# Performance work log

Measured on AMD Instinct MI355X. Metric: run time of the kernel, lower is better.

The kernel has to match this reference:

```python
import jax, jax.numpy as jnp
import numpy as np

HEADS = 12
DIM_HEAD = 64
SCALE = DIM_HEAD ** -0.5


def setup_inputs() -> dict:
    key = jax.random.key(0)
    ks = jax.random.split(key, 7)
    b, n, dim = 16, 1024, 768
    inner = HEADS * DIM_HEAD
    x = jax.random.normal(ks[0], (b, n, dim), dtype=jnp.float32)
    Wq = jax.random.normal(ks[1], (dim, inner), dtype=jnp.float32) * (dim ** -0.5)
    Wkv = jax.random.normal(ks[2], (dim, 2 * inner), dtype=jnp.float32) * (dim ** -0.5)
    mix_pre = jax.random.normal(ks[3], (HEADS, HEADS), dtype=jnp.float32)
    mix_post = jax.random.normal(ks[4], (HEADS, HEADS), dtype=jnp.float32)
    Wo = jax.random.normal(ks[5], (inner, dim), dtype=jnp.float32) * (inner ** -0.5)
    bo = jnp.zeros((dim,), dtype=jnp.float32)
    return {"x": x, "Wq": Wq, "Wkv": Wkv, "mix_pre": mix_pre,
            "mix_post": mix_post, "Wo": Wo, "bo": bo}


def reference(x, Wq, Wkv, mix_pre, mix_post, Wo, bo):
    b, n, dim = x.shape
    h, d = HEADS, DIM_HEAD
    # projections (context is None -> context = x)
    q = (x @ Wq).reshape(b, n, h, d).transpose(0, 2, 1, 3)        # b h n d
    kv = x @ Wkv
    k = kv[..., : h * d].reshape(b, n, h, d).transpose(0, 2, 1, 3)
    v = kv[..., h * d:].reshape(b, n, h, d).transpose(0, 2, 1, 3)
    # scaled QK^T
    attn = jnp.einsum('bhid,bhjd->bhij', q, k) * SCALE             # b h n n
    # talking-heads pre-softmax: mix over head dim
    attn = jnp.einsum('bhij,hg->bgij', attn, mix_pre)
    attn = jax.nn.softmax(attn, axis=-1)
    # talking-heads post-softmax
    attn = jnp.einsum('bhij,hg->bgij', attn, mix_post)
    out = jnp.einsum('bhij,bhjd->bhid', attn, v)                   # b h n d
    out = out.transpose(0, 2, 1, 3).reshape(b, n, h * d)           # b n (h d)
    return out @ Wo + bo
```

## Files before the change

kernel.cpp:

```cpp
#include <hip/hip_runtime.h>


typedef _Float16 f16;
typedef _Float16 f16x8 __attribute__((ext_vector_type(8)));
typedef _Float16 f16x4 __attribute__((ext_vector_type(4)));
typedef float f32x4 __attribute__((ext_vector_type(4)));
typedef float fv4 __attribute__((ext_vector_type(4)));

#define MFMA(a, b, c) __builtin_amdgcn_mfma_f32_16x16x32_f16(a, b, c, 0, 0, 0)

__global__ __launch_bounds__(256) void k_cast_x(const float* __restrict__ x,
                                                f16* __restrict__ xb) {
  int idx = (blockIdx.x * 256 + threadIdx.x) * 8;
  fv4 a = *(const fv4*)(x + idx);
  fv4 b = *(const fv4*)(x + idx + 4);
  f16x8 o;
  o[0] = (f16)a[0]; o[1] = (f16)a[1]; o[2] = (f16)a[2]; o[3] = (f16)a[3];
  o[4] = (f16)b[0]; o[5] = (f16)b[1]; o[6] = (f16)b[2]; o[7] = (f16)b[3];
  *(f16x8*)(xb + idx) = o;
}

__global__ __launch_bounds__(256) void k_prep_w(const float* __restrict__ Wq,
                                                const float* __restrict__ Wkv,
                                                const float* __restrict__ Wo,
                                                f16* __restrict__ Wt,
                                                f16* __restrict__ WoT) {
  int idx = blockIdx.x * 256 + threadIdx.x;
  if (idx < 2304 * 768) {
    int n = idx / 768, k = idx % 768;
    float v = (n < 768) ? Wq[k * 768 + n] * 0.125f
                        : Wkv[k * 1536 + (n - 768)];
    Wt[idx] = (f16)v;
  } else {
    int id2 = idx - 2304 * 768;
    int n = id2 / 768, k = id2 % 768;
    WoT[id2] = (f16)Wo[k * 768 + n];
  }
}

__global__ __launch_bounds__(256) void k_gemm_qkv(const f16* __restrict__ A,
                                                  const f16* __restrict__ Bt,
                                                  f16* __restrict__ qb,
                                                  f16* __restrict__ kb,
                                                  f16* __restrict__ vb) {
  __shared__ f16 As[128 * 72];
  __shared__ f16 Bs[128 * 72];
  const int tid = threadIdx.x;
  const int m0 = blockIdx.y << 7;
  const int n0 = blockIdx.x << 7;
  const int lane = tid & 63, w = tid >> 6;
  const int quad = lane >> 4, col = lane & 15;
  const int wm = (w >> 1) << 6, wn = (w & 1) << 6;
  const f32x4 z4 = {0.f, 0.f, 0.f, 0.f};
  f32x4 acc[4][4];
#pragma unroll
  for (int i = 0; i < 4; ++i)
#pragma unroll
    for (int j = 0; j < 4; ++j) acc[i][j] = z4;

  for (int k0 = 0; k0 < 768; k0 += 64) {
#pragma unroll
    for (int s = 0; s < 4; ++s) {
      int u = s * 256 + tid;
      int row = u >> 3, seg = (u & 7) << 3;
      *(f16x8*)&As[row * 72 + seg] = *(const f16x8*)(A + (m0 + row) * 768 + k0 + seg);
      *(f16x8*)&Bs[row * 72 + seg] = *(const f16x8*)(Bt + (n0 + row) * 768 + k0 + seg);
    }
    __syncthreads();
#pragma unroll
    for (int kk = 0; kk < 64; kk += 32) {
      f16x8 af[4], bf[4];
#pragma unroll
      for (int ic = 0; ic < 4; ++ic)
        af[ic] = *(f16x8*)&As[(wm + ic * 16 + col) * 72 + kk + quad * 8];
#pragma unroll
      for (int jc = 0; jc < 4; ++jc)
        bf[jc] = *(f16x8*)&Bs[(wn + jc * 16 + col) * 72 + kk + quad * 8];
#pragma unroll
      for (int ic = 0; ic < 4; ++ic)
#pragma unroll
        for (int jc = 0; jc < 4; ++jc) acc[ic][jc] = MFMA(af[ic], bf[jc], acc[ic][jc]);
    }
    __syncthreads();
  }
#pragma unroll
  for (int jc = 0; jc < 4; ++jc) {
    int gn = n0 + wn + jc * 16 + col;
#pragma unroll
    for (int ic = 0; ic < 4; ++ic)
#pragma unroll
      for (int r = 0; r < 4; ++r) {
        int gm = m0 + wm + ic * 16 + (quad << 2) + r;
        int b = gm >> 10, i = gm & 1023;
        f16 v = (f16)acc[ic][jc][r];
        if (gn < 768) {
          int h = gn >> 6, dd = gn & 63;
          qb[(((b * 12 + h) << 10) + i) * 64 + dd] = v;
        } else if (gn < 1536) {
          int t = gn - 768; int h = t >> 6, dd = t & 63;
          kb[(((b * 12 + h) << 10) + i) * 64 + dd] = v;
        } else {
          int t = gn - 1536; int h = t >> 6, dd = t & 63;
          vb[(((b * 12 + h) << 10) + i) * 64 + dd] = v;
        }
      }
  }
}

__global__ __launch_bounds__(256) void k_transpose_v(const f16* __restrict__ vb,
                                                     f16* __restrict__ vt) {
  __shared__ f16 t[64 * 72];
  const int bh = blockIdx.x;
  const int n0 = blockIdx.y << 6;
  const int tid = threadIdx.x;
#pragma unroll
  for (int s = 0; s < 2; ++s) {
    int u = s * 256 + tid;
    int r = u >> 3, c = (u & 7) << 3;
    *(f16x8*)&t[r * 72 + c] = *(const f16x8*)(vb + (bh * 1024 + n0 + r) * 64 + c);
  }
  __syncthreads();
#pragma unroll
  for (int s = 0; s < 2; ++s) {
    int u = s * 256 + tid;
    int d = u >> 3, c = (u & 7) << 3;
    f16x8 o;
#pragma unroll
    for (int e = 0; e < 8; ++e) o[e] = t[(c + e) * 72 + d];
    *(f16x8*)(vt + (bh * 64 + d) * 1024 + n0 + c) = o;
  }
}

__global__ __launch_bounds__(256, 2) void k_attn(
    const f16* __restrict__ qb, const f16* __restrict__ kb, const f16* __restrict__ vt,
    const float* __restrict__ mixp, const float* __restrict__ mixq,
    f16* __restrict__ ob) {
  __shared__ f16 Blds[512 * 40];
  __shared__ f16 Pm[16 * 16 * 40];
  __shared__ float m_s[256];
  __shared__ float l_s[256];

  const int tid = threadIdx.x;
  const int bid = blockIdx.x;
  const int b = bid >> 6;
  const int i0 = (bid & 63) << 4;
  const int lane = tid & 63;
  const int w = tid >> 6;
  const int quad = lane >> 4, col = lane & 15;
  const int q4 = quad << 2;
  const int w3 = w * 3, w8 = w * 8, w4 = w << 2;

  {
    f16x8 z8;
#pragma unroll
    for (int e = 0; e < 8; ++e) z8[e] = (f16)0.f;
#pragma unroll
    for (int u = 0; u < 10; ++u) *(f16x8*)&Blds[(tid + u * 256) * 8] = z8;
  }

  f16x8 b_pre, b_post;
#pragma unroll
  for (int e = 0; e < 8; ++e) {
    int hk = quad * 8 + e;
    bool ok = (hk < 12) && (col < 12);
    b_pre[e]  = ok ? (f16)mixp[hk * 12 + col] : (f16)0.f;
    b_post[e] = ok ? (f16)mixq[hk * 12 + col] : (f16)0.f;
  }

  f16x8 qf[3][2];
#pragma unroll
  for (int h3 = 0; h3 < 3; ++h3)
#pragma unroll
    for (int kc = 0; kc < 2; ++kc)
      qf[h3][kc] = *(const f16x8*)(qb + (((b * 12 + w3 + h3) << 10) + i0 + col) * 64 +
                                   kc * 32 + quad * 8);
  __syncthreads();

  auto computeS = [&](int j0, f32x4 (&d1)[8]) {
    const f32x4 z4 = {0.f, 0.f, 0.f, 0.f};
    f32x4 s[3][2];
#pragma unroll
    for (int h3 = 0; h3 < 3; ++h3) {
      s[h3][0] = z4; s[h3][1] = z4;
      const f16* kbase = kb + (((b * 12 + w3 + h3) << 10) + j0) * 64;
#pragma unroll
      for (int js = 0; js < 2; ++js)
#pragma unroll
        for (int kc = 0; kc < 2; ++kc) {
          f16x8 kf = *(const f16x8*)(kbase + (js * 16 + col) * 64 + kc * 32 + quad * 8);
          s[h3][js] = MFMA(qf[h3][kc], kf, s[h3][js]);
        }
    }
#pragma unroll
    for (int h3 = 0; h3 < 3; ++h3)
#pragma unroll
      for (int js = 0; js < 2; ++js)
#pragma unroll
        for (int r = 0; r < 4; ++r)
          Blds[(((q4 + r) << 5) + js * 16 + col) * 40 + w3 + h3] = (f16)s[h3][js][r];
    __syncthreads();
#pragma unroll
    for (int u = 0; u < 8; ++u) {
      f16x8 sf = *(f16x8*)&Blds[((w8 + u) * 16 + col) * 40 + quad * 8];
      d1[u] = MFMA(sf, b_pre, z4);
    }
  };

  float m_run[4], l_run[4];
#pragma unroll
  for (int ii = 0; ii < 4; ++ii) { m_run[ii] = -1e30f; l_run[ii] = 0.f; }

  for (int j0 = 0; j0 < 1024; j0 += 32) {
    f32x4 d1[8];
    computeS(j0, d1);
#pragma unroll
    for (int ii = 0; ii < 4; ++ii) {
      float mx = -1e30f;
#pragma unroll
      for (int uu = 0; uu < 2; ++uu)
#pragma unroll
        for (int r = 0; r < 4; ++r) mx = fmaxf(mx, d1[ii * 2 + uu][r]);
      mx = fmaxf(mx, __shfl_xor(mx, 16));
      mx = fmaxf(mx, __shfl_xor(mx, 32));
      float mnew = fmaxf(m_run[ii], mx);
      float se = 0.f;
#pragma unroll
      for (int uu = 0; uu < 2; ++uu)
#pragma unroll
        for (int r = 0; r < 4; ++r) se += __expf(d1[ii * 2 + uu][r] - mnew);
      se += __shfl_xor(se, 16);
      se += __shfl_xor(se, 32);
      l_run[ii] = l_run[ii] * __expf(m_run[ii] - mnew) + se;
      m_run[ii] = mnew;
    }
    __syncthreads();
  }
  if (quad == 0) {
#pragma unroll
    for (int ii = 0; ii < 4; ++ii) {
      m_s[col * 16 + w4 + ii] = m_run[ii];
      l_s[col * 16 + w4 + ii] = l_run[ii];
    }
  }
  __syncthreads();

  float mv[4], il[4];
#pragma unroll
  for (int ii = 0; ii < 4; ++ii) {
    mv[ii] = m_s[col * 16 + w4 + ii];
    il[ii] = 1.f / l_s[col * 16 + w4 + ii];
  }

  f32x4 oa[3][4];
  {
    const f32x4 z4 = {0.f, 0.f, 0.f, 0.f};
#pragma unroll
    for (int g = 0; g < 3; ++g)
#pragma unroll
      for (int dc = 0; dc < 4; ++dc) oa[g][dc] = z4;
  }

  for (int j0 = 0; j0 < 1024; j0 += 32) {
    f32x4 d1[8];
    computeS(j0, d1);
#pragma unroll
    for (int u = 0; u < 8; ++u) {
      int c0 = (w8 + u) * 16;
      int ii = u >> 1;
#pragma unroll
      for (int r = 0; r < 4; ++r) {
        float P = __expf(d1[u][r] - mv[ii]) * il[ii];
        Blds[(c0 + q4 + r) * 40 + col] = (f16)P;
      }
    }
    f32x4 d2[8];
    {
      const f32x4 z4 = {0.f, 0.f, 0.f, 0.f};
#pragma unroll
      for (int u = 0; u < 8; ++u) {
        f16x8 pf = *(f16x8*)&Blds[((w8 + u) * 16 + col) * 40 + quad * 8];
        d2[u] = MFMA(pf, b_post, z4);
      }
    }
#pragma unroll
    for (int u = 0; u < 8; ++u) {
      int iloc = (w8 + u) >> 1;
      int jbase = ((u & 1) << 4) + q4;
      f16x4 pk;
#pragma unroll
      for (int r = 0; r < 4; ++r) pk[r] = (f16)d2[u][r];
      *(f16x4*)&Pm[(col * 16 + iloc) * 40 + jbase] = pk;
    }
    __syncthreads();
#pragma unroll
    for (int gg = 0; gg < 3; ++gg) {
      int gp = w3 + gg;
      f16x8 af = *(f16x8*)&Pm[(gp * 16 + col) * 40 + quad * 8];
#pragma unroll
      for (int dc = 0; dc < 4; ++dc) {
        f16x8 vf = *(const f16x8*)(vt + (((b * 12 + gp) * 64 + dc * 16 + col) << 10) +
                                   j0 + quad * 8);
        oa[gg][dc] = MFMA(af, vf, oa[gg][dc]);
      }
    }
    __syncthreads();
  }

#pragma unroll
  for (int gg = 0; gg < 3; ++gg) {
    int gp = w3 + gg;
#pragma unroll
    for (int dc = 0; dc < 4; ++dc)
#pragma unroll
      for (int r = 0; r < 4; ++r)
        ob[((b << 10) + i0 + q4 + r) * 768 + gp * 64 + dc * 16 + col] =
            (f16)oa[gg][dc][r];
  }
}

__global__ __launch_bounds__(256) void k_gemm_out(const f16* __restrict__ A,
                                                  const f16* __restrict__ Bt,
                                                  const float* __restrict__ bias,
                                                  float* __restrict__ out) {
  __shared__ f16 As[128 * 72];
  __shared__ f16 Bs[128 * 72];
  const int tid = threadIdx.x;
  const int m0 = blockIdx.y << 7;
  const int n0 = blockIdx.x << 7;
  const int lane = tid & 63, w = tid >> 6;
  const int quad = lane >> 4, col = lane & 15;
  const int wm = (w >> 1) << 6, wn = (w & 1) << 6;
  const f32x4 z4 = {0.f, 0.f, 0.f, 0.f};
  f32x4 acc[4][4];
#pragma unroll
  for (int i = 0; i < 4; ++i)
#pragma unroll
    for (int j = 0; j < 4; ++j) acc[i][j] = z4;

  for (int k0 = 0; k0 < 768; k0 += 64) {
#pragma unroll
    for (int s = 0; s < 4; ++s) {
      int u = s * 256 + tid;
      int row = u >> 3, seg = (u & 7) << 3;
      *(f16x8*)&As[row * 72 + seg] = *(const f16x8*)(A + (m0 + row) * 768 + k0 + seg);
      *(f16x8*)&Bs[row * 72 + seg] = *(const f16x8*)(Bt + (n0 + row) * 768 + k0 + seg);
    }
    __syncthreads();
#pragma unroll
    for (int kk = 0; kk < 64; kk += 32) {
      f16x8 af[4], bf[4];
#pragma unroll
      for (int ic = 0; ic < 4; ++ic)
        af[ic] = *(f16x8*)&As[(wm + ic * 16 + col) * 72 + kk + quad * 8];
#pragma unroll
      for (int jc = 0; jc < 4; ++jc)
        bf[jc] = *(f16x8*)&Bs[(wn + jc * 16 + col) * 72 + kk + quad * 8];
#pragma unroll
      for (int ic = 0; ic < 4; ++ic)
#pragma unroll
        for (int jc = 0; jc < 4; ++jc) acc[ic][jc] = MFMA(af[ic], bf[jc], acc[ic][jc]);
    }
    __syncthreads();
  }
#pragma unroll
  for (int jc = 0; jc < 4; ++jc) {
    int gn = n0 + wn + jc * 16 + col;
    float bv = bias[gn];
#pragma unroll
    for (int ic = 0; ic < 4; ++ic)
#pragma unroll
      for (int r = 0; r < 4; ++r) {
        int gm = m0 + wm + ic * 16 + (quad << 2) + r;
        out[gm * 768 + gn] = acc[ic][jc][r] + bv;
      }
  }
}

extern "C" void kernel_launch(void* const* d_in, const int* in_sizes, int n_in,
                              void* d_out, int out_size, void* d_ws, size_t ws_size,
                              hipStream_t stream) {
  const float* x    = (const float*)d_in[0];
  const float* Wq   = (const float*)d_in[1];
  const float* Wkv  = (const float*)d_in[2];
  const float* mixp = (const float*)d_in[3];
  const float* mixq = (const float*)d_in[4];
  const float* Wo   = (const float*)d_in[5];
  const float* bo   = (const float*)d_in[6];
  float* out = (float*)d_out;

  char* ws = (char*)d_ws;
  f16* xb  = (f16*)(ws);
  f16* Wt  = (f16*)(ws + 25165824);
  f16* WoT = (f16*)(ws + 28704768);
  f16* qb  = (f16*)(ws + 29884416);
  f16* kb  = (f16*)(ws + 55050240);
  f16* vb  = (f16*)(ws + 80216064);
  f16* vt  = xb;
  f16* obuf = vb;

  k_cast_x<<<dim3(6144), dim3(256), 0, stream>>>(x, xb);
  k_prep_w<<<dim3(9216), dim3(256), 0, stream>>>(Wq, Wkv, Wo, Wt, WoT);
  k_gemm_qkv<<<dim3(18, 128), dim3(256), 0, stream>>>(xb, Wt, qb, kb, vb);
  k_transpose_v<<<dim3(192, 16), dim3(256), 0, stream>>>(vb, vt);
  k_attn<<<dim3(1024), dim3(256), 0, stream>>>(qb, kb, vt, mixp, mixq, obuf);
  k_gemm_out<<<dim3(6, 128), dim3(256), 0, stream>>>(obuf, WoT, bo, out);
}
```

Before: 787.1 us.

## Restructure talking-heads attention so each wave owns a key slice across all heads

The attention kernel is reorganized so each wave computes QK^T for all 12 heads over its own 16-key slice of a 64-key tile. The pre/post head-mixing runs on 16x16x16 MFMAs from per-wave LDS, which removes the block-wide barriers in the score stage. The running max is dropped: the first pass only accumulates exp-sums, which assumes mixed logits stay small enough not to overflow. It also adds XOR-swizzled LDS layouts for the mixed probabilities, a remapped block index for locality, and s_setprio around the PV MFMAs, at the cost of keeping query fragments for all 12 heads in registers.

```diff
diff --git a/kernel.cpp b/kernel.cpp
--- a/kernel.cpp
+++ b/kernel.cpp
@@ -8,6 +8,7 @@
 typedef float fv4 __attribute__((ext_vector_type(4)));
 
 #define MFMA(a, b, c) __builtin_amdgcn_mfma_f32_16x16x32_f16(a, b, c, 0, 0, 0)
+#define MFMA16(a, b, c) __builtin_amdgcn_mfma_f32_16x16x16f16(a, b, c, 0, 0, 0)
 
 __global__ __launch_bounds__(256) void k_cast_x(const float* __restrict__ x,
                                                 f16* __restrict__ xb) {
@@ -135,174 +136,149 @@
     const f16* __restrict__ qb, const f16* __restrict__ kb, const f16* __restrict__ vt,
     const float* __restrict__ mixp, const float* __restrict__ mixq,
     f16* __restrict__ ob) {
-  __shared__ f16 Blds[512 * 40];
-  __shared__ f16 Pm[16 * 16 * 40];
-  __shared__ float m_s[256];
-  __shared__ float l_s[256];
+  __shared__ f16 Slds[4][4096];
+  __shared__ f16 Pmb[12 * 16 * 16 * 4];
 
   const int tid = threadIdx.x;
-  const int bid = blockIdx.x;
+  const int bid0 = blockIdx.x;
+  const int bid = ((bid0 & 7) << 7) | (bid0 >> 3);
   const int b = bid >> 6;
   const int i0 = (bid & 63) << 4;
   const int lane = tid & 63;
   const int w = tid >> 6;
   const int quad = lane >> 4, col = lane & 15;
   const int q4 = quad << 2;
-  const int w3 = w * 3, w8 = w * 8, w4 = w << 2;
-
-  {
-    f16x8 z8;
-#pragma unroll
-    for (int e = 0; e < 8; ++e) z8[e] = (f16)0.f;
-#pragma unroll
-    for (int u = 0; u < 10; ++u) *(f16x8*)&Blds[(tid + u * 256) * 8] = z8;
-  }
-
-  f16x8 b_pre, b_post;
-#pragma unroll
-  for (int e = 0; e < 8; ++e) {
-    int hk = quad * 8 + e;
+  const int w3 = w * 3;
+  const int jw = w << 4;
+  const f32x4 z4 = {0.f, 0.f, 0.f, 0.f};
+
+  f16x4 b_pre, b_post;
+#pragma unroll
+  for (int e = 0; e < 4; ++e) {
+    int hk = q4 + e;
     bool ok = (hk < 12) && (col < 12);
     b_pre[e]  = ok ? (f16)mixp[hk * 12 + col] : (f16)0.f;
     b_post[e] = ok ? (f16)mixq[hk * 12 + col] : (f16)0.f;
   }
 
-  f16x8 qf[3][2];
-#pragma unroll
-  for (int h3 = 0; h3 < 3; ++h3)
+  f16* Sw = &Slds[w][0];
+  {
+    f16x4 z; z[0] = (f16)0.f; z[1] = (f16)0.f; z[2] = (f16)0.f; z[3] = (f16)0.f;
+#pragma unroll
+    for (int u = 0; u < 4; ++u) {
+      int idx = u * 64 + lane;
+      *(f16x4*)&Sw[(((idx >> 4) << 6) + 48 + (idx & 15)) * 4] = z;
+    }
+  }
+
+  f16x8 qf[12][2];
+#pragma unroll
+  for (int h = 0; h < 12; ++h)
 #pragma unroll
     for (int kc = 0; kc < 2; ++kc)
-      qf[h3][kc] = *(const f16x8*)(qb + (((b * 12 + w3 + h3) << 10) + i0 + col) * 64 +
-                                   kc * 32 + quad * 8);
+      qf[h][kc] = *(const f16x8*)(qb + ((((b * 12 + h) << 10) + i0 + col) << 6) +
+                                  kc * 32 + quad * 8);
+
+  auto stage = [&](int j0) {
+#pragma unroll
+    for (int hg = 0; hg < 3; ++hg) {
+      f32x4 s4[4];
+#pragma unroll
+      for (int e = 0; e < 4; ++e) {
+        int h = hg * 4 + e;
+        const f16* kbase = kb + ((((b * 12 + h) << 10) + j0 + jw + col) << 6);
+        f16x8 kf0 = *(const f16x8*)(kbase + quad * 8);
+        f16x8 kf1 = *(const f16x8*)(kbase + 32 + quad * 8);
+        f32x4 a = MFMA(qf[h][0], kf0, z4);
+        s4[e] = MFMA(qf[h][1], kf1, a);
+      }
+#pragma unroll
+      for (int r = 0; r < 4; ++r) {
+        f16x4 p;
+        p[0] = (f16)s4[0][r]; p[1] = (f16)s4[1][r];
+        p[2] = (f16)s4[2][r]; p[3] = (f16)s4[3][r];
+        *(f16x4*)&Sw[((col << 6) + hg * 16 + ((q4 + r + col) & 15)) * 4] = p;
+      }
+    }
+  };
+
+  float l_run[4] = {0.f, 0.f, 0.f, 0.f};
+  for (int j0 = 0; j0 < 1024; j0 += 64) {
+    stage(j0);
+#pragma unroll
+    for (int t = 0; t < 16; ++t) {
+      f16x4 sB = *(const f16x4*)&Sw[((t << 6) + quad * 16 + ((col + t) & 15)) * 4];
+      f32x4 d1 = MFMA16(b_pre, sB, z4);
+#pragma unroll
+      for (int r = 0; r < 4; ++r) l_run[r] += __expf(d1[r]);
+    }
+  }
+  float* Lb = (float*)Pmb;
+#pragma unroll
+  for (int r = 0; r < 4; ++r) Lb[(w * 16 + q4 + r) * 16 + col] = l_run[r];
   __syncthreads();
-
-  auto computeS = [&](int j0, f32x4 (&d1)[8]) {
-    const f32x4 z4 = {0.f, 0.f, 0.f, 0.f};
-    f32x4 s[3][2];
-#pragma unroll
-    for (int h3 = 0; h3 < 3; ++h3) {
-      s[h3][0] = z4; s[h3][1] = z4;
-      const f16* kbase = kb + (((b * 12 + w3 + h3) << 10) + j0) * 64;
-#pragma unroll
-      for (int js = 0; js < 2; ++js)
-#pragma unroll
-        for (int kc = 0; kc < 2; ++kc) {
-          f16x8 kf = *(const f16x8*)(kbase + (js * 16 + col) * 64 + kc * 32 + quad * 8);
-          s[h3][js] = MFMA(qf[h3][kc], kf, s[h3][js]);
+  float il[4];
+#pragma unroll
+  for (int r = 0; r < 4; ++r) {
+    float s = 0.f;
+#pragma unroll
+    for (int ww = 0; ww < 4; ++ww) s += Lb[(ww * 16 + q4 + r) * 16 + col];
+    il[r] = 1.f / s;
+  }
+  __syncthreads();
+
+  f32x4 oa[3][4];
+#pragma unroll
+  for (int g = 0; g < 3; ++g)
+#pragma unroll
+    for (int dc = 0; dc < 4; ++dc) oa[g][dc] = z4;
+
+  for (int j0 = 0; j0 < 1024; j0 += 64) {
+    stage(j0);
+#pragma unroll
+    for (int tt = 0; tt < 4; ++tt) {
+      f16x4 pk[4];
+#pragma unroll
+      for (int t4 = 0; t4 < 4; ++t4) {
+        int t = tt * 4 + t4;
+        f16x4 sB = *(const f16x4*)&Sw[((t << 6) + quad * 16 + ((col + t) & 15)) * 4];
+        f32x4 d1 = MFMA16(b_pre, sB, z4);
+        f16x4 pA;
+#pragma unroll
+        for (int r = 0; r < 4; ++r) pA[r] = (f16)(__expf(d1[r]) * il[r]);
+        f32x4 d2 = MFMA16(pA, b_post, z4);
+#pragma unroll
+        for (int r = 0; r < 4; ++r) pk[r][t4] = (f16)d2[r];
+      }
+      if (col < 12) {
+#pragma unroll
+        for (int r = 0; r < 4; ++r) {
+          int k4 = (col + q4 + r) & 15;
+          *(f16x4*)&Pmb[(((col << 4) + q4 + r) * 16 + ((w * 4 + tt) ^ k4)) * 4] = pk[r];
         }
-    }
-#pragma unroll
-    for (int h3 = 0; h3 < 3; ++h3)
-#pragma unroll
-      for (int js = 0; js < 2; ++js)
-#pragma unroll
-        for (int r = 0; r < 4; ++r)
-          Blds[(((q4 + r) << 5) + js * 16 + col) * 40 + w3 + h3] = (f16)s[h3][js][r];
-    __syncthreads();
-#pragma unroll
-    for (int u = 0; u < 8; ++u) {
-      f16x8 sf = *(f16x8*)&Blds[((w8 + u) * 16 + col) * 40 + quad * 8];
-      d1[u] = MFMA(sf, b_pre, z4);
-    }
-  };
-
-  float m_run[4], l_run[4];
-#pragma unroll
-  for (int ii = 0; ii < 4; ++ii) { m_run[ii] = -1e30f; l_run[ii] = 0.f; }
-
-  for (int j0 = 0; j0 < 1024; j0 += 32) {
-    f32x4 d1[8];
-    computeS(j0, d1);
-#pragma unroll
-    for (int ii = 0; ii < 4; ++ii) {
-      float mx = -1e30f;
-#pragma unroll
-      for (int uu = 0; uu < 2; ++uu)
-#pragma unroll
-        for (int r = 0; r < 4; ++r) mx = fmaxf(mx, d1[ii * 2 + uu][r]);
-      mx = fmaxf(mx, __shfl_xor(mx, 16));
-      mx = fmaxf(mx, __shfl_xor(mx, 32));
-      float mnew = fmaxf(m_run[ii], mx);
-      float se = 0.f;
-#pragma unroll
-      for (int uu = 0; uu < 2; ++uu)
-#pragma unroll
-        for (int r = 0; r < 4; ++r) se += __expf(d1[ii * 2 + uu][r] - mnew);
-      se += __shfl_xor(se, 16);
-      se += __shfl_xor(se, 32);
-      l_run[ii] = l_run[ii] * __expf(m_run[ii] - mnew) + se;
-      m_run[ii] = mnew;
-    }
-    __syncthreads();
-  }
-  if (quad == 0) {
-#pragma unroll
-    for (int ii = 0; ii < 4; ++ii) {
-      m_s[col * 16 + w4 + ii] = m_run[ii];
-      l_s[col * 16 + w4 + ii] = l_run[ii];
-    }
-  }
-  __syncthreads();
-
-  float mv[4], il[4];
-#pragma unroll
-  for (int ii = 0; ii < 4; ++ii) {
-    mv[ii] = m_s[col * 16 + w4 + ii];
-    il[ii] = 1.f / l_s[col * 16 + w4 + ii];
-  }
-
-  f32x4 oa[3][4];
-  {
-    const f32x4 z4 = {0.f, 0.f, 0.f, 0.f};
-#pragma unroll
-    for (int g = 0; g < 3; ++g)
-#pragma unroll
-      for (int dc = 0; dc < 4; ++dc) oa[g][dc] = z4;
-  }
-
-  for (int j0 = 0; j0 < 1024; j0 += 32) {
-    f32x4 d1[8];
-    computeS(j0, d1);
-#pragma unroll
-    for (int u = 0; u < 8; ++u) {
-      int c0 = (w8 + u) * 16;
-      int ii = u >> 1;
-#pragma unroll
-      for (int r = 0; r < 4; ++r) {
-        float P = __expf(d1[u][r] - mv[ii]) * il[ii];
-        Blds[(c0 + q4 + r) * 40 + col] = (f16)P;
-      }
-    }
-    f32x4 d2[8];
-    {
-      const f32x4 z4 = {0.f, 0.f, 0.f, 0.f};
-#pragma unroll
-      for (int u = 0; u < 8; ++u) {
-        f16x8 pf = *(f16x8*)&Blds[((w8 + u) * 16 + col) * 40 + quad * 8];
-        d2[u] = MFMA(pf, b_post, z4);
-      }
-    }
-#pragma unroll
-    for (int u = 0; u < 8; ++u) {
-      int iloc = (w8 + u) >> 1;
-      int jbase = ((u & 1) << 4) + q4;
-      f16x4 pk;
-#pragma unroll
-      for (int r = 0; r < 4; ++r) pk[r] = (f16)d2[u][r];
-      *(f16x4*)&Pm[(col * 16 + iloc) * 40 + jbase] = pk;
-    }
-    __syncthreads();
+      }
+    }
+    __syncthreads();
+    __builtin_amdgcn_s_setprio(1);
 #pragma unroll
     for (int gg = 0; gg < 3; ++gg) {
       int gp = w3 + gg;
-      f16x8 af = *(f16x8*)&Pm[(gp * 16 + col) * 40 + quad * 8];
-#pragma unroll
-      for (int dc = 0; dc < 4; ++dc) {
-        f16x8 vf = *(const f16x8*)(vt + (((b * 12 + gp) * 64 + dc * 16 + col) << 10) +
-                                   j0 + quad * 8);
-        oa[gg][dc] = MFMA(af, vf, oa[gg][dc]);
-      }
-    }
+      int k4r = (gp + col) & 15;
+#pragma unroll
+      for (int jh = 0; jh < 2; ++jh) {
+        int ub = (jh * 4 + quad) * 2;
+        f16x4 lo = *(const f16x4*)&Pmb[(((gp << 4) + col) * 16 + (ub ^ k4r)) * 4];
+        f16x4 hi = *(const f16x4*)&Pmb[(((gp << 4) + col) * 16 + ((ub + 1) ^ k4r)) * 4];
+        f16x8 aP = __builtin_shufflevector(lo, hi, 0, 1, 2, 3, 4, 5, 6, 7);
+#pragma unroll
+        for (int dc = 0; dc < 4; ++dc) {
+          f16x8 vf = *(const f16x8*)(vt + ((((b * 12 + gp) << 6) + dc * 16 + col) << 10) +
+                                     j0 + jh * 32 + quad * 8);
+          oa[gg][dc] = MFMA(aP, vf, oa[gg][dc]);
+        }
+      }
+    }
+    __builtin_amdgcn_s_setprio(0);
     __syncthreads();
   }
 
```

New measurement: 827.8 us. 1.05x slower.
